# Optimization experiments

Measured on AMD Instinct MI355X. Metric: run time of the kernel, lower is better.

The kernel has to match this reference:

```python
import jax, jax.numpy as jnp
import numpy as np

N = 100000

def gcn_conv(x, src, dst, W, b, n):
    # x: [N, Fin]; src/dst: [E'] (self-loops already included); W: [Fin, Fout]
    h = x @ W  # [N, Fout]
    deg = jax.ops.segment_sum(jnp.ones_like(dst, dtype=h.dtype), dst, num_segments=n)  # [N]
    dinv = deg ** -0.5  # deg >= 1 due to self-loops
    norm = dinv[src] * dinv[dst]  # [E']
    msg = h[src] * norm[:, None]  # gather + scale, [E', Fout]
    out = jax.ops.segment_sum(msg, dst, num_segments=n)  # scatter-add to targets
    return out + b

def setup_inputs() -> dict:
    key = jax.random.key(0)
    k1, k2, k3, k4, k5, k6 = jax.random.split(key, 6)
    x = jax.random.normal(k1, (N, 128), dtype=jnp.float32)
    edge_index = jax.random.randint(k2, (2, 1600000), 0, N, dtype=jnp.int32)
    W1 = jax.random.normal(k3, (128, 64), dtype=jnp.float32) * 0.1
    b1 = jnp.zeros((64,), dtype=jnp.float32)
    W2 = jax.random.normal(k4, (64, 41), dtype=jnp.float32) * 0.1
    b2 = jnp.zeros((41,), dtype=jnp.float32)
    return {"x": x, "edge_index": edge_index, "W1": W1, "b1": b1, "W2": W2, "b2": b2}

def reference(x, edge_index, W1, b1, W2, b2):
    n = x.shape[0]
    loops = jnp.arange(n, dtype=edge_index.dtype)
    src = jnp.concatenate([edge_index[0], loops])  # add self-loops (PyG gcn_norm default)
    dst = jnp.concatenate([edge_index[1], loops])
    # dropout is identity in eval mode (self.training=False)
    h = gcn_conv(x, src, dst, W1, b1, n)
    h = jax.nn.relu(h)
    out = gcn_conv(h, src, dst, W2, b2, n)
    return out
```

## Files before the change

kernel.cpp:

```cpp
#include <hip/hip_runtime.h>


#define FIN 128
#define F1  64
#define F2  41
#define FP  64

#define BSH    8
#define BCAP   6144
#define NBMAX  512
#define CHUNK_P 4096

#define MT 128
#define KC 16

#define SMEM_BYTES 29952

__device__ __forceinline__ unsigned short f2bf(float f) {
    unsigned u = __builtin_bit_cast(unsigned, f);
    u += 0x7FFFu + ((u >> 16) & 1u);
    return (unsigned short)(u >> 16);
}
__device__ __forceinline__ float bf2f(unsigned short h) {
    unsigned u = ((unsigned)h) << 16;
    return __builtin_bit_cast(float, u);
}

__global__ __launch_bounds__(256) void k_partmm1(
    const int* __restrict__ src, const int* __restrict__ dst,
    int* __restrict__ gcur, int* __restrict__ pairs, int E, int nchunks,
    const float* __restrict__ x, const float* __restrict__ W1,
    unsigned short* __restrict__ hs, int n) {
    __shared__ alignas(16) char smem[SMEM_BYTES];
    int tid = threadIdx.x;
    if ((int)blockIdx.x < nchunks) {
        int* hist = (int*)smem;
        int* gsh  = hist + NBMAX;
        int* lex  = gsh + NBMAX;
        int* stot = lex + 256;
        int* limg = stot + 4;
        unsigned short* bid = (unsigned short*)(limg + CHUNK_P);
        int e0  = blockIdx.x * CHUNK_P;
        int ds[CHUNK_P / 256], ss[CHUNK_P / 256];
#pragma unroll
        for (int j = 0; j < CHUNK_P / 256; j++) {
            int e = e0 + j * 256 + tid;
            if (e < E) { ds[j] = dst[e]; ss[j] = src[e]; } else ds[j] = -1;
        }
        hist[tid] = 0; hist[tid + 256] = 0;
        __syncthreads();
#pragma unroll
        for (int j = 0; j < CHUNK_P / 256; j++)
            if (ds[j] >= 0) atomicAdd(&hist[ds[j] >> BSH], 1);
        __syncthreads();
        int b0 = 2 * tid, b1 = 2 * tid + 1;
        int c0 = hist[b0], c1 = hist[b1];
        int s  = c0 + c1;
        lex[tid] = s;
        __syncthreads();
        for (int off = 1; off < 256; off <<= 1) {
            int v = lex[tid];
            int a = (tid >= off) ? lex[tid - off] : 0;
            __syncthreads();
            lex[tid] = v + a;
            __syncthreads();
        }
        int incl = lex[tid];
        if (tid == 255) stot[0] = incl;
        int ex = incl - s;
        int g0 = c0 ? atomicAdd(&gcur[b0], c0) : 0;
        int g1 = c1 ? atomicAdd(&gcur[b1], c1) : 0;
        hist[b0] = ex; hist[b1] = ex + c0;
        gsh[b0]  = b0 * BCAP + g0 - ex;
        gsh[b1]  = b1 * BCAP + g1 - (ex + c0);
        __syncthreads();
#pragma unroll
        for (int j = 0; j < CHUNK_P / 256; j++) {
            if (ds[j] >= 0) {
                int b = ds[j] >> BSH;
                int p = atomicAdd(&hist[b], 1);
                limg[p] = (ss[j] << BSH) | (ds[j] & 255);
                bid[p]  = (unsigned short)b;
            }
        }
        __syncthreads();
        int tot = stot[0];
        for (int k = tid; k < tot; k += 256)
            pairs[k + gsh[bid[k]]] = limg[k];
    } else {
        unsigned short* Ws = (unsigned short*)smem;
        float (*As)[MT] = (float(*)[MT])(smem + FIN * F1 * 2);
        int n0 = ((int)blockIdx.x - nchunks) * MT;
#pragma unroll
        for (int j = 0; j < 8; j++) {
            int f = j * 256 + tid;
            float4 w4 = ((const float4*)W1)[f];
            ushort4 o = { f2bf(w4.x), f2bf(w4.y), f2bf(w4.z), f2bf(w4.w) };
            ((ushort4*)Ws)[f] = o;
        }
        int m0 = (tid & 15) * 8;
        int c0 = (tid >> 4) * 4;
        int m_l = tid & 127;
        int kh  = (tid >> 7) * 8;
        bool mvalid = (n0 + m_l) < n;
        const float* xrow = x + (size_t)(n0 + m_l) * FIN + kh;
        float acc[8][4] = {};
        for (int kc = 0; kc < FIN; kc += KC) {
            __syncthreads();
            float4 v0 = mvalid ? *(const float4*)(xrow + kc)     : float4{0.f,0.f,0.f,0.f};
            float4 v1 = mvalid ? *(const float4*)(xrow + kc + 4) : float4{0.f,0.f,0.f,0.f};
            As[kh + 0][m_l] = v0.x; As[kh + 1][m_l] = v0.y;
            As[kh + 2][m_l] = v0.z; As[kh + 3][m_l] = v0.w;
            As[kh + 4][m_l] = v1.x; As[kh + 5][m_l] = v1.y;
            As[kh + 6][m_l] = v1.z; As[kh + 7][m_l] = v1.w;
            __syncthreads();
#pragma unroll
            for (int k = 0; k < KC; k++) {
                float4 a0 = *(const float4*)&As[k][m0];
                float4 a1 = *(const float4*)&As[k][m0 + 4];
                ushort4 wq = *(const ushort4*)&Ws[(kc + k) * F1 + c0];
                float wx = bf2f(wq.x), wy = bf2f(wq.y);
                float wz = bf2f(wq.z), ww = bf2f(wq.w);
                float a[8] = {a0.x, a0.y, a0.z, a0.w, a1.x, a1.y, a1.z, a1.w};
#pragma unroll
                for (int i = 0; i < 8; i++) {
                    acc[i][0] += a[i] * wx;
                    acc[i][1] += a[i] * wy;
                    acc[i][2] += a[i] * wz;
                    acc[i][3] += a[i] * ww;
                }
            }
        }
#pragma unroll
        for (int i = 0; i < 8; i++) {
            int node = n0 + m0 + i;
            if (node < n) {
                ushort4 o = { f2bf(acc[i][0]), f2bf(acc[i][1]),
                              f2bf(acc[i][2]), f2bf(acc[i][3]) };
                *(ushort4*)&hs[((size_t)node << 6) + c0] = o;
            }
        }
    }
}

__global__ __launch_bounds__(256) void k_build(
    const int* __restrict__ gcur, const int* __restrict__ pairs,
    int* __restrict__ adjcur, int* __restrict__ adj,
    int2* __restrict__ rowinfo, float* __restrict__ dinv,
    unsigned short* __restrict__ hs1, int n) {
    __shared__ int lcnt[256];
    __shared__ int lex[256];
    __shared__ int lcur[256];
    __shared__ int ladj[BCAP];
    __shared__ float ldv[256];
    __shared__ int sbase;
    int tid = threadIdx.x;
    int b   = blockIdx.x;
    int cntb  = gcur[b]; if (cntb > BCAP) cntb = BCAP;
    int node0 = b << BSH;
    const int* pb = pairs + (size_t)b * BCAP;

    if (tid == 0) sbase = atomicAdd(adjcur, cntb);
    lcnt[tid] = 0;
    __syncthreads();
    for (int k = tid; k < cntb; k += 256) atomicAdd(&lcnt[pb[k] & 255], 1);
    __syncthreads();
    int own = lcnt[tid];
    lex[tid] = own;
    __syncthreads();
    for (int off = 1; off < 256; off <<= 1) {
        int val = lex[tid];
        int add = (tid >= off) ? lex[tid - off] : 0;
        __syncthreads();
        lex[tid] = val + add;
        __syncthreads();
    }
    int excl = lex[tid] - own;
    __syncthreads();
    lcur[tid] = excl;
    float dvn = rsqrtf((float)own + 1.0f);
    ldv[tid]  = dvn;
    __syncthreads();
    for (int k = tid; k < cntb; k += 256) {
        int pk  = pb[k];
        int pos = atomicAdd(&lcur[pk & 255], 1);
        ladj[pos] = pk >> BSH;
    }
    __syncthreads();
    int base = sbase;
    for (int k = tid; k < cntb; k += 256) adj[base + k] = ladj[k];
    int node = node0 + tid;
    if (node < n) {
        rowinfo[node] = make_int2(base + excl, own);
        dinv[node]    = dvn;
    }
    for (int u = tid; u < 2048; u += 256) {
        int nd = node0 + (u >> 3);
        if (nd >= n) break;
        float dv = ldv[u >> 3];
        ushort4* p = (ushort4*)&hs1[((size_t)nd << 6) + (u & 7) * 8];
        ushort4 a = p[0], c = p[1];
        a.x = f2bf(bf2f(a.x) * dv); a.y = f2bf(bf2f(a.y) * dv);
        a.z = f2bf(bf2f(a.z) * dv); a.w = f2bf(bf2f(a.w) * dv);
        c.x = f2bf(bf2f(c.x) * dv); c.y = f2bf(bf2f(c.y) * dv);
        c.z = f2bf(bf2f(c.z) * dv); c.w = f2bf(bf2f(c.w) * dv);
        p[0] = a; p[1] = c;
    }
}

__global__ __launch_bounds__(256) void k_agg1(
    const int2* __restrict__ rowinfo, const int* __restrict__ adj,
    const unsigned short* __restrict__ hs, const float* __restrict__ dinv,
    const float* __restrict__ b1, unsigned short* __restrict__ h1b, int n, int E) {
    int node = blockIdx.x * 4 + (threadIdx.x >> 6);
    if (node >= n) return;
    int lane = threadIdx.x & 63;
    int grp  = lane >> 4;
    int p4   = (lane & 15) * 4;
    int2 ri = rowinfo[node];
    int beg = ri.x, deg = ri.y;
    float4 acc = {0.f, 0.f, 0.f, 0.f};
    if (grp == 0) {
        ushort4 u = *(const ushort4*)&hs[((size_t)node << 6) + p4];
        acc.x = bf2f(u.x); acc.y = bf2f(u.y); acc.z = bf2f(u.z); acc.w = bf2f(u.w);
    }
    for (int base = 0; base < deg; base += 64) {
        int m = deg - base; if (m > 64) m = 64;
        int idx = beg + base + lane;
        int myoff = adj[idx < E ? idx : 0] << 6;
        int e = 0;
        for (; e + 16 <= m; e += 16) {
            int o0 = __shfl(myoff, e + grp),      o1 = __shfl(myoff, e + 4 + grp);
            int o2 = __shfl(myoff, e + 8 + grp),  o3 = __shfl(myoff, e + 12 + grp);
            ushort4 u0 = *(const ushort4*)&hs[(size_t)o0 + p4];
            ushort4 u1 = *(const ushort4*)&hs[(size_t)o1 + p4];
            ushort4 u2 = *(const ushort4*)&hs[(size_t)o2 + p4];
            ushort4 u3 = *(const ushort4*)&hs[(size_t)o3 + p4];
            acc.x += (bf2f(u0.x) + bf2f(u1.x)) + (bf2f(u2.x) + bf2f(u3.x));
            acc.y += (bf2f(u0.y) + bf2f(u1.y)) + (bf2f(u2.y) + bf2f(u3.y));
            acc.z += (bf2f(u0.z) + bf2f(u1.z)) + (bf2f(u2.z) + bf2f(u3.z));
            acc.w += (bf2f(u0.w) + bf2f(u1.w)) + (bf2f(u2.w) + bf2f(u3.w));
        }
        for (; e < m; e += 4) {
            int sl = e + grp;
            int o = __shfl(myoff, sl);
            if (sl < m) {
                ushort4 u = *(const ushort4*)&hs[(size_t)o + p4];
                acc.x += bf2f(u.x); acc.y += bf2f(u.y);
                acc.z += bf2f(u.z); acc.w += bf2f(u.w);
            }
        }
    }
    acc.x += __shfl_xor(acc.x, 16); acc.y += __shfl_xor(acc.y, 16);
    acc.z += __shfl_xor(acc.z, 16); acc.w += __shfl_xor(acc.w, 16);
    acc.x += __shfl_xor(acc.x, 32); acc.y += __shfl_xor(acc.y, 32);
    acc.z += __shfl_xor(acc.z, 32); acc.w += __shfl_xor(acc.w, 32);
    if (grp == 0) {
        float dvn = dinv[node];
        float4 bg = *(const float4*)&b1[p4];
        float vx = acc.x * dvn + bg.x; vx = vx > 0.f ? vx : 0.f;
        float vy = acc.y * dvn + bg.y; vy = vy > 0.f ? vy : 0.f;
        float vz = acc.z * dvn + bg.z; vz = vz > 0.f ? vz : 0.f;
        float vw = acc.w * dvn + bg.w; vw = vw > 0.f ? vw : 0.f;
        ushort4 o = { f2bf(vx), f2bf(vy), f2bf(vz), f2bf(vw) };
        *(ushort4*)&h1b[((size_t)node << 6) + p4] = o;
    }
}

__global__ __launch_bounds__(256) void k_mm2(
    const unsigned short* __restrict__ h1b, const float* __restrict__ W2,
    const float* __restrict__ dinv, unsigned short* __restrict__ hs2, int n) {
    __shared__ float Ws[F1 * FP];
    __shared__ float As[KC][MT];
    int t  = threadIdx.x;
    int n0 = blockIdx.x * MT;
    for (int idx = t; idx < F1 * FP; idx += 256) {
        int k = idx >> 6, c = idx & 63;
        Ws[idx] = (c < F2) ? W2[k * F2 + c] : 0.f;
    }
    int m0 = (t & 15) * 8;
    int c0 = (t >> 4) * 4;
    int m_l = t & 127;
    int kh  = (t >> 7) * 8;
    bool mvalid = (n0 + m_l) < n;
    const unsigned short* hrow = h1b + ((size_t)(n0 + m_l) << 6) + kh;
    float acc[8][4] = {};
    for (int kc = 0; kc < F1; kc += KC) {
        __syncthreads();
        ushort4 u0 = mvalid ? *(const ushort4*)(hrow + kc)     : ushort4{0,0,0,0};
        ushort4 u1 = mvalid ? *(const ushort4*)(hrow + kc + 4) : ushort4{0,0,0,0};
        As[kh + 0][m_l] = bf2f(u0.x); As[kh + 1][m_l] = bf2f(u0.y);
        As[kh + 2][m_l] = bf2f(u0.z); As[kh + 3][m_l] = bf2f(u0.w);
        As[kh + 4][m_l] = bf2f(u1.x); As[kh + 5][m_l] = bf2f(u1.y);
        As[kh + 6][m_l] = bf2f(u1.z); As[kh + 7][m_l] = bf2f(u1.w);
        __syncthreads();
#pragma unroll
        for (int k = 0; k < KC; k++) {
            float4 a0 = *(const float4*)&As[k][m0];
            float4 a1 = *(const float4*)&As[k][m0 + 4];
            float4 w  = *(const float4*)&Ws[(kc + k) * FP + c0];
            float a[8] = {a0.x, a0.y, a0.z, a0.w, a1.x, a1.y, a1.z, a1.w};
#pragma unroll
            for (int i = 0; i < 8; i++) {
                acc[i][0] += a[i] * w.x;
                acc[i][1] += a[i] * w.y;
                acc[i][2] += a[i] * w.z;
                acc[i][3] += a[i] * w.w;
            }
        }
    }
#pragma unroll
    for (int i = 0; i < 8; i++) {
        int node = n0 + m0 + i;
        if (node < n) {
            float dv = dinv[node];
            ushort4 o = { f2bf(acc[i][0] * dv), f2bf(acc[i][1] * dv),
                          f2bf(acc[i][2] * dv), f2bf(acc[i][3] * dv) };
            *(ushort4*)&hs2[((size_t)node << 6) + c0] = o;
        }
    }
}

__global__ __launch_bounds__(256) void k_agg2(
    const int2* __restrict__ rowinfo, const int* __restrict__ adj,
    const unsigned short* __restrict__ hs2, const float* __restrict__ dinv,
    const float* __restrict__ b2, float* __restrict__ out, int n, int E) {
    int node = blockIdx.x * 4 + (threadIdx.x >> 6);
    if (node >= n) return;
    int lane = threadIdx.x & 63;
    int grp  = lane >> 4;
    int p4   = (lane & 15) * 4;
    int2 ri = rowinfo[node];
    int beg = ri.x, deg = ri.y;
    float4 acc = {0.f, 0.f, 0.f, 0.f};
    if (grp == 0) {
        ushort4 u = *(const ushort4*)&hs2[((size_t)node << 6) + p4];
        acc.x = bf2f(u.x); acc.y = bf2f(u.y); acc.z = bf2f(u.z); acc.w = bf2f(u.w);
    }
    for (int base = 0; base < deg; base += 64) {
        int m = deg - base; if (m > 64) m = 64;
        int idx = beg + base + lane;
        int myoff = adj[idx < E ? idx : 0] << 6;
        int e = 0;
        for (; e + 16 <= m; e += 16) {
            int o0 = __shfl(myoff, e + grp),      o1 = __shfl(myoff, e + 4 + grp);
            int o2 = __shfl(myoff, e + 8 + grp),  o3 = __shfl(myoff, e + 12 + grp);
            ushort4 u0 = *(const ushort4*)&hs2[(size_t)o0 + p4];
            ushort4 u1 = *(const ushort4*)&hs2[(size_t)o1 + p4];
            ushort4 u2 = *(const ushort4*)&hs2[(size_t)o2 + p4];
            ushort4 u3 = *(const ushort4*)&hs2[(size_t)o3 + p4];
            acc.x += (bf2f(u0.x) + bf2f(u1.x)) + (bf2f(u2.x) + bf2f(u3.x));
            acc.y += (bf2f(u0.y) + bf2f(u1.y)) + (bf2f(u2.y) + bf2f(u3.y));
            acc.z += (bf2f(u0.z) + bf2f(u1.z)) + (bf2f(u2.z) + bf2f(u3.z));
            acc.w += (bf2f(u0.w) + bf2f(u1.w)) + (bf2f(u2.w) + bf2f(u3.w));
        }
        for (; e < m; e += 4) {
            int sl = e + grp;
            int o = __shfl(myoff, sl);
            if (sl < m) {
                ushort4 u = *(const ushort4*)&hs2[(size_t)o + p4];
                acc.x += bf2f(u.x); acc.y += bf2f(u.y);
                acc.z += bf2f(u.z); acc.w += bf2f(u.w);
            }
        }
    }
    acc.x += __shfl_xor(acc.x, 16); acc.y += __shfl_xor(acc.y, 16);
    acc.z += __shfl_xor(acc.z, 16); acc.w += __shfl_xor(acc.w, 16);
    acc.x += __shfl_xor(acc.x, 32); acc.y += __shfl_xor(acc.y, 32);
    acc.z += __shfl_xor(acc.z, 32); acc.w += __shfl_xor(acc.w, 32);
    if (grp == 0) {
        float dv = dinv[node];
        float vv[4] = {acc.x, acc.y, acc.z, acc.w};
#pragma unroll
        for (int j = 0; j < 4; j++) {
            int f = p4 + j;
            if (f < F2) out[(size_t)node * F2 + f] = vv[j] * dv + b2[f];
        }
    }
}

extern "C" void kernel_launch(void* const* d_in, const int* in_sizes, int n_in,
                              void* d_out, int out_size, void* d_ws, size_t ws_size,
                              hipStream_t stream) {
    const float* x  = (const float*)d_in[0];
    const int*   ei = (const int*)d_in[1];
    const float* W1 = (const float*)d_in[2];
    const float* b1 = (const float*)d_in[3];
    const float* W2 = (const float*)d_in[4];
    const float* b2 = (const float*)d_in[5];
    float* out = (float*)d_out;

    const int n = in_sizes[0] / FIN;
    const int E = in_sizes[1] / 2;
    const int* src = ei;
    const int* dst = ei + E;
    const int nbuck   = (n + 255) >> BSH;
    const int nchunks = (E + CHUNK_P - 1) / CHUNK_P;
    const int nmm     = (n + MT - 1) / MT;
    const int nagg    = (n + 3) / 4;

    char* ws = (char*)d_ws;
    size_t off = 0;
    auto alloc = [&](size_t bytes) {
        void* p = ws + off;
        off = (off + bytes + 511) & ~(size_t)511;
        return p;
    };
    int*   gcur    = (int*)alloc((size_t)(NBMAX + 1) * 4);
    int*   pairs   = (int*)alloc((size_t)nbuck * BCAP * 4);
    int*   adj     = (int*)alloc((size_t)E * 4);
    int2*  rowinfo = (int2*)alloc((size_t)n * 8);
    float* dinv    = (float*)alloc((size_t)n * 4);
    unsigned short* hs1 = (unsigned short*)alloc((size_t)n * FP * 2);
    unsigned short* hs2 = (unsigned short*)alloc((size_t)n * FP * 2);
    unsigned short* h1b = (unsigned short*)alloc((size_t)n * FP * 2);

    hipMemsetAsync(gcur, 0, (size_t)(NBMAX + 1) * 4, stream);
    k_partmm1<<<nchunks + nmm, 256, 0, stream>>>(src, dst, gcur, pairs, E, nchunks,
                                                 x, W1, hs1, n);
    k_build<<<nbuck, 256, 0, stream>>>(gcur, pairs, gcur + NBMAX, adj, rowinfo,
                                       dinv, hs1, n);
    k_agg1<<<nagg, 256, 0, stream>>>(rowinfo, adj, hs1, dinv, b1, h1b, n, E);
    k_mm2<<<nmm, 256, 0, stream>>>(h1b, W2, dinv, hs2, n);
    k_agg2<<<nagg, 256, 0, stream>>>(rowinfo, adj, hs2, dinv, b2, out, n, E);
}
```

Baseline: 283.8 us.

## Replace global-atomic bucket partition with per-chunk offset tables read by build

The partition kernel no longer reserves bucket space through global atomics. Each chunk writes its locally sorted pairs contiguously and records per-bucket offsets in a 16-bit table, which also removes the memset. The build kernel then walks every chunk's segment for its bucket, so each thread makes serial, poorly coalesced reads across about 400 chunks. It also scatters adj directly into a fixed BCAP-strided layout instead of staging it in shared memory and compacting with an atomic base.

```diff
diff --git a/kernel.cpp b/kernel.cpp
--- a/kernel.cpp
+++ b/kernel.cpp
@@ -8,13 +8,12 @@
 
 #define BSH    8
 #define BCAP   6144
-#define NBMAX  512
 #define CHUNK_P 4096
 
 #define MT 128
 #define KC 16
 
-#define SMEM_BYTES 29952
+#define SMEM_BYTES 24576
 
 __device__ __forceinline__ unsigned short f2bf(float f) {
     unsigned u = __builtin_bit_cast(unsigned, f);
@@ -28,18 +27,16 @@
 
 __global__ __launch_bounds__(256) void k_partmm1(
     const int* __restrict__ src, const int* __restrict__ dst,
-    int* __restrict__ gcur, int* __restrict__ pairs, int E, int nchunks,
+    unsigned short* __restrict__ offs, int* __restrict__ pairs,
+    int E, int nchunks, int NB,
     const float* __restrict__ x, const float* __restrict__ W1,
     unsigned short* __restrict__ hs, int n) {
     __shared__ alignas(16) char smem[SMEM_BYTES];
     int tid = threadIdx.x;
     if ((int)blockIdx.x < nchunks) {
         int* hist = (int*)smem;
-        int* gsh  = hist + NBMAX;
-        int* lex  = gsh + NBMAX;
-        int* stot = lex + 256;
-        int* limg = stot + 4;
-        unsigned short* bid = (unsigned short*)(limg + CHUNK_P);
+        int* lex  = hist + 512;
+        int* limg = lex + 256;
         int e0  = blockIdx.x * CHUNK_P;
         int ds[CHUNK_P / 256], ss[CHUNK_P / 256];
 #pragma unroll
@@ -66,13 +63,13 @@
             __syncthreads();
         }
         int incl = lex[tid];
-        if (tid == 255) stot[0] = incl;
-        int ex = incl - s;
-        int g0 = c0 ? atomicAdd(&gcur[b0], c0) : 0;
-        int g1 = c1 ? atomicAdd(&gcur[b1], c1) : 0;
-        hist[b0] = ex; hist[b1] = ex + c0;
-        gsh[b0]  = b0 * BCAP + g0 - ex;
-        gsh[b1]  = b1 * BCAP + g1 - (ex + c0);
+        int ex0 = incl - s;
+        int ex1 = ex0 + c0;
+        unsigned short* orow = offs + (size_t)blockIdx.x * (NB + 1);
+        if (b0 < NB) orow[b0] = (unsigned short)ex0;
+        if (b1 < NB) orow[b1] = (unsigned short)ex1;
+        if (tid == 255) orow[NB] = (unsigned short)incl;
+        hist[b0] = ex0; hist[b1] = ex1;
         __syncthreads();
 #pragma unroll
         for (int j = 0; j < CHUNK_P / 256; j++) {
@@ -80,13 +77,13 @@
                 int b = ds[j] >> BSH;
                 int p = atomicAdd(&hist[b], 1);
                 limg[p] = (ss[j] << BSH) | (ds[j] & 255);
-                bid[p]  = (unsigned short)b;
-            }
-        }
-        __syncthreads();
-        int tot = stot[0];
+            }
+        }
+        __syncthreads();
+        int tot = lex[255];
+        int* pout = pairs + (size_t)blockIdx.x * CHUNK_P;
         for (int k = tid; k < tot; k += 256)
-            pairs[k + gsh[bid[k]]] = limg[k];
+            pout[k] = limg[k];
     } else {
         unsigned short* Ws = (unsigned short*)smem;
         float (*As)[MT] = (float(*)[MT])(smem + FIN * F1 * 2);
@@ -144,26 +141,28 @@
 }
 
 __global__ __launch_bounds__(256) void k_build(
-    const int* __restrict__ gcur, const int* __restrict__ pairs,
-    int* __restrict__ adjcur, int* __restrict__ adj,
+    const unsigned short* __restrict__ offs, const int* __restrict__ pairs,
+    int nchunks, int NB, int* __restrict__ adj,
     int2* __restrict__ rowinfo, float* __restrict__ dinv,
     unsigned short* __restrict__ hs1, int n) {
     __shared__ int lcnt[256];
     __shared__ int lex[256];
     __shared__ int lcur[256];
-    __shared__ int ladj[BCAP];
     __shared__ float ldv[256];
-    __shared__ int sbase;
     int tid = threadIdx.x;
     int b   = blockIdx.x;
-    int cntb  = gcur[b]; if (cntb > BCAP) cntb = BCAP;
+    int NB1 = NB + 1;
     int node0 = b << BSH;
-    const int* pb = pairs + (size_t)b * BCAP;
-
-    if (tid == 0) sbase = atomicAdd(adjcur, cntb);
+    int base  = b * BCAP;
+
     lcnt[tid] = 0;
     __syncthreads();
-    for (int k = tid; k < cntb; k += 256) atomicAdd(&lcnt[pb[k] & 255], 1);
+    for (int c = tid; c < nchunks; c += 256) {
+        int s0 = offs[(size_t)c * NB1 + b];
+        int s1 = offs[(size_t)c * NB1 + b + 1];
+        const int* pc = pairs + (size_t)c * CHUNK_P;
+        for (int i = s0; i < s1; i++) atomicAdd(&lcnt[pc[i] & 255], 1);
+    }
     __syncthreads();
     int own = lcnt[tid];
     lex[tid] = own;
@@ -176,19 +175,20 @@
         __syncthreads();
     }
     int excl = lex[tid] - own;
-    __syncthreads();
+    float dvn = rsqrtf((float)own + 1.0f);
     lcur[tid] = excl;
-    float dvn = rsqrtf((float)own + 1.0f);
     ldv[tid]  = dvn;
     __syncthreads();
-    for (int k = tid; k < cntb; k += 256) {
-        int pk  = pb[k];
-        int pos = atomicAdd(&lcur[pk & 255], 1);
-        ladj[pos] = pk >> BSH;
-    }
-    __syncthreads();
-    int base = sbase;
-    for (int k = tid; k < cntb; k += 256) adj[base + k] = ladj[k];
+    for (int c = tid; c < nchunks; c += 256) {
+        int s0 = offs[(size_t)c * NB1 + b];
+        int s1 = offs[(size_t)c * NB1 + b + 1];
+        const int* pc = pairs + (size_t)c * CHUNK_P;
+        for (int i = s0; i < s1; i++) {
+            int pk  = pc[i];
+            int pos = atomicAdd(&lcur[pk & 255], 1);
+            adj[base + pos] = pk >> BSH;
+        }
+    }
     int node = node0 + tid;
     if (node < n) {
         rowinfo[node] = make_int2(base + excl, own);
@@ -211,7 +211,7 @@
 __global__ __launch_bounds__(256) void k_agg1(
     const int2* __restrict__ rowinfo, const int* __restrict__ adj,
     const unsigned short* __restrict__ hs, const float* __restrict__ dinv,
-    const float* __restrict__ b1, unsigned short* __restrict__ h1b, int n, int E) {
+    const float* __restrict__ b1, unsigned short* __restrict__ h1b, int n, int AT) {
     int node = blockIdx.x * 4 + (threadIdx.x >> 6);
     if (node >= n) return;
     int lane = threadIdx.x & 63;
@@ -227,7 +227,7 @@
     for (int base = 0; base < deg; base += 64) {
         int m = deg - base; if (m > 64) m = 64;
         int idx = beg + base + lane;
-        int myoff = adj[idx < E ? idx : 0] << 6;
+        int myoff = adj[idx < AT ? idx : 0] << 6;
         int e = 0;
         for (; e + 16 <= m; e += 16) {
             int o0 = __shfl(myoff, e + grp),      o1 = __shfl(myoff, e + 4 + grp);
@@ -324,7 +324,7 @@
 __global__ __launch_bounds__(256) void k_agg2(
     const int2* __restrict__ rowinfo, const int* __restrict__ adj,
     const unsigned short* __restrict__ hs2, const float* __restrict__ dinv,
-    const float* __restrict__ b2, float* __restrict__ out, int n, int E) {
+    const float* __restrict__ b2, float* __restrict__ out, int n, int AT) {
     int node = blockIdx.x * 4 + (threadIdx.x >> 6);
     if (node >= n) return;
     int lane = threadIdx.x & 63;
@@ -340,7 +340,7 @@
     for (int base = 0; base < deg; base += 64) {
         int m = deg - base; if (m > 64) m = 64;
         int idx = beg + base + lane;
-        int myoff = adj[idx < E ? idx : 0] << 6;
+        int myoff = adj[idx < AT ? idx : 0] << 6;
         int e = 0;
         for (; e + 16 <= m; e += 16) {
             int o0 = __shfl(myoff, e + grp),      o1 = __shfl(myoff, e + 4 + grp);
@@ -398,6 +398,7 @@
     const int nchunks = (E + CHUNK_P - 1) / CHUNK_P;
     const int nmm     = (n + MT - 1) / MT;
     const int nagg    = (n + 3) / 4;
+    const int adjtot  = nbuck * BCAP;
 
     char* ws = (char*)d_ws;
     size_t off = 0;
@@ -406,21 +407,20 @@
         off = (off + bytes + 511) & ~(size_t)511;
         return p;
     };
-    int*   gcur    = (int*)alloc((size_t)(NBMAX + 1) * 4);
-    int*   pairs   = (int*)alloc((size_t)nbuck * BCAP * 4);
-    int*   adj     = (int*)alloc((size_t)E * 4);
+    unsigned short* offs = (unsigned short*)alloc((size_t)nchunks * (nbuck + 1) * 2);
+    int*   pairs   = (int*)alloc((size_t)nchunks * CHUNK_P * 4);
+    int*   adj     = (int*)alloc((size_t)adjtot * 4 + 256);
     int2*  rowinfo = (int2*)alloc((size_t)n * 8);
     float* dinv    = (float*)alloc((size_t)n * 4);
     unsigned short* hs1 = (unsigned short*)alloc((size_t)n * FP * 2);
     unsigned short* hs2 = (unsigned short*)alloc((size_t)n * FP * 2);
     unsigned short* h1b = (unsigned short*)alloc((size_t)n * FP * 2);
 
-    hipMemsetAsync(gcur, 0, (size_t)(NBMAX + 1) * 4, stream);
-    k_partmm1<<<nchunks + nmm, 256, 0, stream>>>(src, dst, gcur, pairs, E, nchunks,
-                                                 x, W1, hs1, n);
-    k_build<<<nbuck, 256, 0, stream>>>(gcur, pairs, gcur + NBMAX, adj, rowinfo,
+    k_partmm1<<<nchunks + nmm, 256, 0, stream>>>(src, dst, offs, pairs, E, nchunks,
+                                                 nbuck, x, W1, hs1, n);
+    k_build<<<nbuck, 256, 0, stream>>>(offs, pairs, nchunks, nbuck, adj, rowinfo,
                                        dinv, hs1, n);
-    k_agg1<<<nagg, 256, 0, stream>>>(rowinfo, adj, hs1, dinv, b1, h1b, n, E);
+    k_agg1<<<nagg, 256, 0, stream>>>(rowinfo, adj, hs1, dinv, b1, h1b, n, adjtot);
     k_mm2<<<nmm, 256, 0, stream>>>(h1b, W2, dinv, hs2, n);
-    k_agg2<<<nagg, 256, 0, stream>>>(rowinfo, adj, hs2, dinv, b2, out, n, E);
-}
+    k_agg2<<<nagg, 256, 0, stream>>>(rowinfo, adj, hs2, dinv, b2, out, n, adjtot);
+}
```

Result: slower. 293.7 us (+3.5%).
